# Performance work log

Measured on AMD Instinct MI355X. Metric: run time of the kernel, lower is better.

## Reference

```python
import jax, jax.numpy as jnp
import numpy as np
import math

N, E, H, NB, NL, NG, NELEM = 50000, 800000, 64, 8, 2, 64, 100
CUTOFF = 5.0


def _lin(k, fin, fout):
    kw, kb = jax.random.split(k)
    bound = 1.0 / math.sqrt(fin)
    w = jax.random.uniform(kw, (fin, fout), jnp.float32, -bound, bound)
    b = jax.random.uniform(kb, (fout,), jnp.float32, -bound, bound)
    return w, b


def setup_inputs() -> dict:
    key = jax.random.key(0)
    ks = jax.random.split(key, 12)
    z = jax.random.randint(ks[0], (N,), 0, NELEM)
    pos = jax.random.normal(ks[1], (N, 3), jnp.float32)
    edge_index = jax.random.randint(ks[2], (2, E), 0, N)
    batch = jnp.sort(jax.random.randint(ks[3], (N,), 0, NG))
    embed = jax.random.normal(ks[4], (NELEM, H), jnp.float32)
    # stacked per-interaction MLP params, leading dim = NL
    msg_w1, msg_b1, msg_w2, msg_b2 = [], [], [], []
    upd_w1, upd_b1, upd_w2, upd_b2 = [], [], [], []
    for l in range(NL):
        kl = jax.random.fold_in(ks[5], l)
        k1, k2, k3, k4 = jax.random.split(kl, 4)
        w, b = _lin(k1, 2 * H + NB, H); msg_w1.append(w); msg_b1.append(b)
        w, b = _lin(k2, H, H); msg_w2.append(w); msg_b2.append(b)
        w, b = _lin(k3, 2 * H, H); upd_w1.append(w); upd_b1.append(b)
        w, b = _lin(k4, H, H); upd_w2.append(w); upd_b2.append(b)
    eh_w1, eh_b1 = _lin(ks[6], H, H)
    eh_w2, eh_b2 = _lin(ks[7], H, 1)
    return {
        "z": z, "pos": pos, "edge_index": edge_index, "batch": batch,
        "embed": embed,
        "msg_w1": jnp.stack(msg_w1), "msg_b1": jnp.stack(msg_b1),
        "msg_w2": jnp.stack(msg_w2), "msg_b2": jnp.stack(msg_b2),
        "upd_w1": jnp.stack(upd_w1), "upd_b1": jnp.stack(upd_b1),
        "upd_w2": jnp.stack(upd_w2), "upd_b2": jnp.stack(upd_b2),
        "eh_w1": eh_w1, "eh_b1": eh_b1, "eh_w2": eh_w2, "eh_b2": eh_b2,
    }


def _mace_energy(pos, embed, msg_w1, msg_b1, msg_w2, msg_b2,
                 upd_w1, upd_b1, upd_w2, upd_b2,
                 eh_w1, eh_b1, eh_w2, eh_b2,
                 z, edge_index, batch):
    row, col = edge_index[0], edge_index[1]
    edge_vec = pos[row] - pos[col]                      # (E,3)
    d = jnp.linalg.norm(edge_vec, axis=-1)              # (E,)
    env = jnp.where(d < CUTOFF,
                    jnp.cos(d * (math.pi / (2 * CUTOFF))) ** 2,
                    0.0)
    freqs = jnp.arange(1, NB + 1, dtype=pos.dtype) * (math.pi / CUTOFF)
    d_safe = jnp.where(d > 0, d, 1.0)[:, None]
    edge_attr = jnp.sin(freqs * d[:, None]) / d_safe * env[:, None]  # (E,NB)

    x = embed[z]                                        # (N,H)
    for l in range(NL):
        # PyG source_to_target: x_j = x[row], x_i = x[col], aggregate at col
        msg_in = jnp.concatenate([x[col], x[row], edge_attr], axis=-1)  # (E,2H+NB)
        m = jax.nn.silu(msg_in @ msg_w1[l] + msg_b1[l]) @ msg_w2[l] + msg_b2[l]
        agg = jax.ops.segment_sum(m, col, num_segments=N)               # (N,H)
        u_in = jnp.concatenate([x, agg], axis=-1)
        upd = jax.nn.silu(u_in @ upd_w1[l] + upd_b1[l]) @ upd_w2[l] + upd_b2[l]
        x = x + upd

    atomic_e = jax.nn.silu(x @ eh_w1 + eh_b1) @ eh_w2 + eh_b2           # (N,1)
    energy = jax.ops.segment_sum(atomic_e, batch, num_segments=NG)      # (NG,1)
    return energy.squeeze(-1)


def reference(z, pos, edge_index, batch, embed,
              msg_w1, msg_b1, msg_w2, msg_b2,
              upd_w1, upd_b1, upd_w2, upd_b2,
              eh_w1, eh_b1, eh_w2, eh_b2):
    return _mace_energy(pos, embed, msg_w1, msg_b1, msg_w2, msg_b2,
                        upd_w1, upd_b1, upd_w2, upd_b2,
                        eh_w1, eh_b1, eh_w2, eh_b2,
                        z, edge_index, batch)
```

## Files before the change

kernel.cpp:

```cpp
#include <hip/hip_runtime.h>
#include <math.h>

#define NN 50000
#define EE 800000
#define HH 64
#define NBASIS 8
#define NLAYER 2
#define NGRAPH 64
#define NBLK1 49

using half2_t = decltype(__builtin_amdgcn_cvt_pkrtz(0.0f, 0.0f));
typedef _Float16 f16x8 __attribute__((ext_vector_type(8)));
typedef float f32x4 __attribute__((ext_vector_type(4)));

union U4H8 { uint4 u; f16x8 h; };

__device__ __forceinline__ float silu_f(float v) {
    return v * (1.0f / (1.0f + __expf(-v)));
}

__device__ __forceinline__ unsigned pk2(float a, float b) {
    union { half2_t h; unsigned u; } x;
    x.h = __builtin_amdgcn_cvt_pkrtz(a, b);
    return x.u;
}

__global__ __launch_bounds__(256) void prep_k(
    const int* __restrict__ z, const float* __restrict__ embed,
    float* __restrict__ x, unsigned* __restrict__ xh,
    const float* __restrict__ msg_w1, const float* __restrict__ msg_w2,
    const float* __restrict__ upd_w1, const float* __restrict__ upd_w2,
    const float* __restrict__ eh_w1,
    unsigned* __restrict__ w1t, unsigned* __restrict__ w2t,
    unsigned* __restrict__ w1tu, unsigned* __restrict__ w2tu,
    unsigned* __restrict__ ehw1t,
    const int* __restrict__ ecol, int* __restrict__ deg)
{
    int b = blockIdx.x;
    if (b < 6250) {
        int idx = b * 256 + threadIdx.x;
        int n = idx >> 5;
        int p = idx & 31;
        const float2* er = (const float2*)(embed + ((size_t)z[n] << 6));
        float2 v = er[p];
        ((float2*)x)[idx] = v;
        xh[idx] = pk2(v.x, v.y);
    } else if (b < 6362) {
        int idx = (b - 6250) * 256 + threadIdx.x;
        if (idx < 10240) {
            int l = idx / 5120, rem = idx % 5120;
            int f = rem / 80, kp = rem % 80;
            const float* w = msg_w1 + (size_t)l * 136 * 64;
            unsigned v = 0;
            if (kp < 68) v = pk2(w[(2*kp)*64 + f], w[(2*kp+1)*64 + f]);
            w1t[idx] = v;
        } else if (idx < 14336) {
            int j = idx - 10240;
            int l = j / 2048, rem = j % 2048;
            int n = rem / 32, kp = rem % 32;
            const float* w = msg_w2 + (size_t)l * 64 * 64;
            w2t[j] = pk2(w[(2*kp)*64 + n], w[(2*kp+1)*64 + n]);
        } else if (idx < 22528) {
            int j = idx - 14336;
            int l = j / 4096, rem = j % 4096;
            int f = rem >> 6, kp = rem & 63;
            const float* w = upd_w1 + (size_t)l * 128 * 64;
            w1tu[j] = pk2(w[(2*kp)*64 + f], w[(2*kp+1)*64 + f]);
        } else if (idx < 26624) {
            int j = idx - 22528;
            int l = j / 2048, rem = j % 2048;
            int n = rem / 32, kp = rem % 32;
            const float* w = upd_w2 + (size_t)l * 64 * 64;
            w2tu[j] = pk2(w[(2*kp)*64 + n], w[(2*kp+1)*64 + n]);
        } else if (idx < 28672) {
            int j = idx - 26624;
            int f = j / 32, kp = j % 32;
            ehw1t[j] = pk2(eh_w1[(2*kp)*64 + f], eh_w1[(2*kp+1)*64 + f]);
        }
    } else {
        int e = (b - 6362) * 256 + threadIdx.x;
        if (e < EE) atomicAdd(&deg[ecol[e]], 1);
    }
}

__global__ __launch_bounds__(1024) void scan1_k(
    const int* __restrict__ deg, int* __restrict__ cursor,
    int* __restrict__ bsum)
{
    __shared__ int wsum[16];
    int t = threadIdx.x, lane = t & 63, wave = t >> 6;
    int i = blockIdx.x * 1024 + t;
    int v = (i < NN) ? deg[i] : 0;
    int s = v;
#pragma unroll
    for (int off = 1; off < 64; off <<= 1) {
        int tv = __shfl_up(s, off, 64);
        if (lane >= off) s += tv;
    }
    if (lane == 63) wsum[wave] = s;
    __syncthreads();
    if (wave == 0) {
        int ws = (lane < 16) ? wsum[lane] : 0;
        int ss = ws;
#pragma unroll
        for (int off = 1; off < 16; off <<= 1) {
            int tv = __shfl_up(ss, off, 64);
            if (lane >= off) ss += tv;
        }
        if (lane < 16) wsum[lane] = ss - ws;
    }
    __syncthreads();
    int excl = wsum[wave] + s - v;
    if (i < NN) cursor[i] = excl;
    if (t == 1023) bsum[blockIdx.x] = excl + v;
}

__global__ __launch_bounds__(64) void scan2_k(int* __restrict__ bsum)
{
    int lane = threadIdx.x;
    int v = (lane < NBLK1) ? bsum[lane] : 0;
    int s = v;
#pragma unroll
    for (int off = 1; off < 64; off <<= 1) {
        int tv = __shfl_up(s, off, 64);
        if (lane >= off) s += tv;
    }
    if (lane < NBLK1) bsum[lane] = s - v;
}

__global__ __launch_bounds__(256) void scatter_k(
    const int* __restrict__ erow, const int* __restrict__ ecol,
    const float* __restrict__ pos,
    int* __restrict__ cursor, const int* __restrict__ bsum,
    uint4* __restrict__ edgeS)
{
    int e = blockIdx.x * 256 + threadIdx.x;
    if (e >= EE) return;
    int c = ecol[e], r = erow[e];
    int slot = atomicAdd(&cursor[c], 1) + bsum[c >> 10];
    float dx = pos[3*r]   - pos[3*c];
    float dy = pos[3*r+1] - pos[3*c+1];
    float dz = pos[3*r+2] - pos[3*c+2];
    float d = sqrtf(dx*dx + dy*dy + dz*dz);
    uint4 v;
    v.x = (unsigned)r; v.y = (unsigned)c;
    v.z = __float_as_uint(d); v.w = 0;
    edgeS[slot] = v;
}

__global__ __launch_bounds__(256, 4) void msg_k(
    const uint4* __restrict__ edgeS,
    const unsigned* __restrict__ xh,
    const unsigned* __restrict__ w1t, const float* __restrict__ b1,
    const unsigned* __restrict__ w2t, const float* __restrict__ b2,
    float* __restrict__ agg)
{
    __shared__ __align__(16) unsigned earr[4][64 * 4];
    __shared__ int ckey_s[4][64];
    __shared__ int rkey_s[4][64];
    __shared__ float Mbuf[4][64 * 33];

    const int wid  = threadIdx.x >> 6;
    const int lane = threadIdx.x & 63;
    const int q = lane >> 4, n15 = lane & 15;
    const size_t base = (size_t)blockIdx.x * 256 + wid * 64;

    int mykey;
    {
        uint4 ev = edgeS[base + lane];
        rkey_s[wid][lane] = (int)ev.x;
        mykey = (int)ev.y;
        ckey_s[wid][lane] = mykey;
        float d = __uint_as_float(ev.z);
        float env = 0.0f;
        if (d < 5.0f) {
            float cv = __cosf(d * 0.31415926535897932f);
            env = cv * cv;
        }
        float scale = (d > 0.0f) ? (env / d) : env;
        float ea[NBASIS];
#pragma unroll
        for (int k = 0; k < NBASIS; ++k)
            ea[k] = __sinf((float)(k + 1) * 0.62831853071795865f * d) * scale;
#pragma unroll
        for (int p = 0; p < 4; ++p)
            earr[wid][lane * 4 + p] = pk2(ea[2*p], ea[2*p+1]);
    }
    int pkk = __shfl_up(mykey, 1, 64);
    unsigned long long bmask = __ballot(lane > 0 && mykey != pkk);
    unsigned m32 = (unsigned)(bmask >> (lane & 32));
    __syncthreads();

    int cn[4], rn[4];
#pragma unroll
    for (int nt = 0; nt < 4; ++nt) {
        int eB = nt * 16 + n15;
        cn[nt] = ckey_s[wid][eB];
        rn[nt] = rkey_s[wid][eB];
    }

    f32x4 acc1[4][4];
#pragma unroll
    for (int mt = 0; mt < 4; ++mt) {
        f32x4 binit = *(const f32x4*)(b1 + mt * 16 + q * 4);
#pragma unroll
        for (int nt = 0; nt < 4; ++nt) acc1[mt][nt] = binit;
    }
#pragma unroll
    for (int ks = 0; ks < 5; ++ks) {
        U4H8 bfk[4];
#pragma unroll
        for (int nt = 0; nt < 4; ++nt) {
            if (ks == 4) {
                uint4 zz; zz.x = zz.y = zz.z = zz.w = 0;
                bfk[nt].u = (q == 0) ? *(const uint4*)(earr[wid] + (nt * 16 + n15) * 4) : zz;
            } else if (ks < 2) {
                bfk[nt].u = ((const uint4*)(xh + ((size_t)cn[nt] << 5)))[ks * 4 + q];
            } else {
                bfk[nt].u = ((const uint4*)(xh + ((size_t)rn[nt] << 5)))[(ks - 2) * 4 + q];
            }
        }
#pragma unroll
        for (int mt = 0; mt < 4; ++mt) {
            U4H8 af;
            af.u = *(const uint4*)(w1t + (size_t)(mt * 16 + n15) * 80 + ks * 16 + q * 4);
#pragma unroll
            for (int nt = 0; nt < 4; ++nt)
                acc1[mt][nt] = __builtin_amdgcn_mfma_f32_16x16x32_f16(
                    af.h, bfk[nt].h, acc1[mt][nt], 0, 0, 0);
        }
    }

    unsigned psrc[4][4][2];
#pragma unroll
    for (int mt = 0; mt < 4; ++mt)
#pragma unroll
        for (int nt = 0; nt < 4; ++nt) {
            psrc[mt][nt][0] = pk2(silu_f(acc1[mt][nt][0]), silu_f(acc1[mt][nt][1]));
            psrc[mt][nt][1] = pk2(silu_f(acc1[mt][nt][2]), silu_f(acc1[mt][nt][3]));
        }

    f32x4 acc2[4][4];
#pragma unroll
    for (int nt = 0; nt < 4; ++nt) {
        float b2v = b2[nt * 16 + n15];
        f32x4 binit; binit[0] = b2v; binit[1] = b2v; binit[2] = b2v; binit[3] = b2v;
#pragma unroll
        for (int et = 0; et < 4; ++et) acc2[et][nt] = binit;
    }
#pragma unroll
    for (int ks2 = 0; ks2 < 2; ++ks2) {
        U4H8 wb[4];
#pragma unroll
        for (int nt = 0; nt < 4; ++nt)
            wb[nt].u = *(const uint4*)(w2t + (size_t)(nt * 16 + n15) * 32 + ks2 * 16 + q * 4);
#pragma unroll
        for (int et = 0; et < 4; ++et) {
            unsigned tmp[4];
#pragma unroll
            for (int jr = 0; jr < 4; ++jr) {
                int srcl = (2 * (q & 1) + (jr >> 1)) * 16 + n15;
                unsigned v0 = (unsigned)__shfl((int)psrc[2 * ks2][et][jr & 1], srcl, 64);
                unsigned v1 = (unsigned)__shfl((int)psrc[2 * ks2 + 1][et][jr & 1], srcl, 64);
                tmp[jr] = (q >> 1) ? v1 : v0;
            }
            U4H8 pf;
            pf.u.x = tmp[0]; pf.u.y = tmp[1]; pf.u.z = tmp[2]; pf.u.w = tmp[3];
#pragma unroll
            for (int nt = 0; nt < 4; ++nt)
                acc2[et][nt] = __builtin_amdgcn_mfma_f32_16x16x32_f16(
                    pf.h, wb[nt].h, acc2[et][nt], 0, 0, 0);
        }
    }

#pragma unroll
    for (int hf = 0; hf < 2; ++hf) {
#pragma unroll
        for (int et = 0; et < 4; ++et)
#pragma unroll
            for (int t2 = 0; t2 < 2; ++t2) {
                int nt = 2 * hf + t2;
                int cl = t2 * 16 + n15;
                int eb = et * 16 + q * 4;
#pragma unroll
                for (int r = 0; r < 4; ++r)
                    Mbuf[wid][(eb + r) * 33 + cl] = acc2[et][nt][r];
            }
        __syncthreads();
        {
            int cl = lane & 31, st = lane >> 5;
            int ebase = 32 * st;
            float run = Mbuf[wid][ebase * 33 + cl];
            int runkey = ckey_s[wid][ebase];
            bool atstart = true;
#pragma unroll
            for (int i = 1; i < 32; ++i) {
                float v = Mbuf[wid][(ebase + i) * 33 + cl];
                if ((m32 >> i) & 1u) {
                    float* dst = agg + ((size_t)runkey << 6) + hf * 32 + cl;
                    if (atstart) atomicAdd(dst, run); else *dst = run;
                    runkey = ckey_s[wid][ebase + i]; atstart = false;
                    run = v;
                } else {
                    run += v;
                }
            }
            atomicAdd(agg + ((size_t)runkey << 6) + hf * 32 + cl, run);
        }
        __syncthreads();
    }
}

__global__ __launch_bounds__(256) void upd_k(
    float* __restrict__ x, unsigned* __restrict__ xh,
    float* __restrict__ agg,
    const unsigned* __restrict__ w1t, const float* __restrict__ b1,
    const unsigned* __restrict__ w2t, const float* __restrict__ b2,
    const unsigned* __restrict__ ehw1t, const float* __restrict__ ehb1,
    const float* __restrict__ ehw2, const float* __restrict__ ehb2,
    const int* __restrict__ batch, float* __restrict__ energy,
    int do_zero, int do_head)
{
    __shared__ unsigned MU[4][16 * 33];
    __shared__ float esum[NGRAPH];

    const int tid = threadIdx.x;
    const int wid = tid >> 6;
    const int lane = tid & 63;
    const int q = lane >> 4, n15 = lane & 15;
    const int base16 = blockIdx.x * 64 + wid * 16;

    if (do_head) {
        if (tid < NGRAPH) esum[tid] = 0.0f;
        __syncthreads();
    }

    int nodeB = base16 + n15;
    int ncB = (nodeB < NN) ? nodeB : (NN - 1);

    f32x4 acc1[4];
#pragma unroll
    for (int mt = 0; mt < 4; ++mt)
        acc1[mt] = *(const f32x4*)(b1 + mt * 16 + q * 4);
#pragma unroll
    for (int ks = 0; ks < 4; ++ks) {
        U4H8 bfk;
        if (ks < 2) {
            bfk.u = ((const uint4*)(xh + ((size_t)ncB << 5)))[ks * 4 + q];
        } else {
            const float4* ap = (const float4*)(agg + ((size_t)ncB << 6));
            int o = (ks - 2) * 8 + 2 * q;
            float4 a0 = ap[o], a1 = ap[o + 1];
            bfk.u.x = pk2(a0.x, a0.y); bfk.u.y = pk2(a0.z, a0.w);
            bfk.u.z = pk2(a1.x, a1.y); bfk.u.w = pk2(a1.z, a1.w);
        }
#pragma unroll
        for (int mt = 0; mt < 4; ++mt) {
            U4H8 af;
            af.u = *(const uint4*)(w1t + (size_t)(mt * 16 + n15) * 64 + ks * 16 + q * 4);
            acc1[mt] = __builtin_amdgcn_mfma_f32_16x16x32_f16(
                af.h, bfk.h, acc1[mt], 0, 0, 0);
        }
    }

    unsigned psrc[4][2];
#pragma unroll
    for (int mt = 0; mt < 4; ++mt) {
        psrc[mt][0] = pk2(silu_f(acc1[mt][0]), silu_f(acc1[mt][1]));
        psrc[mt][1] = pk2(silu_f(acc1[mt][2]), silu_f(acc1[mt][3]));
    }

    f32x4 acc2[4];
#pragma unroll
    for (int nt = 0; nt < 4; ++nt) {
        float b2v = b2[nt * 16 + n15];
        acc2[nt][0] = b2v; acc2[nt][1] = b2v; acc2[nt][2] = b2v; acc2[nt][3] = b2v;
    }
#pragma unroll
    for (int ks2 = 0; ks2 < 2; ++ks2) {
        unsigned tmp[4];
#pragma unroll
        for (int jr = 0; jr < 4; ++jr) {
            int srcl = (2 * (q & 1) + (jr >> 1)) * 16 + n15;
            unsigned v0 = (unsigned)__shfl((int)psrc[2 * ks2][jr & 1], srcl, 64);
            unsigned v1 = (unsigned)__shfl((int)psrc[2 * ks2 + 1][jr & 1], srcl, 64);
            tmp[jr] = (q >> 1) ? v1 : v0;
        }
        U4H8 pf;
        pf.u.x = tmp[0]; pf.u.y = tmp[1]; pf.u.z = tmp[2]; pf.u.w = tmp[3];
#pragma unroll
        for (int nt = 0; nt < 4; ++nt) {
            U4H8 wb;
            wb.u = *(const uint4*)(w2t + (size_t)(nt * 16 + n15) * 32 + ks2 * 16 + q * 4);
            acc2[nt] = __builtin_amdgcn_mfma_f32_16x16x32_f16(
                pf.h, wb.h, acc2[nt], 0, 0, 0);
        }
    }

#pragma unroll
    for (int nt = 0; nt < 4; ++nt) {
#pragma unroll
        for (int r = 0; r < 4; ++r) {
            int node = base16 + 4 * q + r;
            float vnew = 0.0f;
            if (node < NN) {
                float* xp = x + ((size_t)node << 6) + nt * 16 + n15;
                vnew = *xp + acc2[nt][r];
                *xp = vnew;
            }
            float vpart = __shfl_xor(vnew, 1, 64);
            if ((n15 & 1) == 0) {
                unsigned pv = pk2(vnew, vpart);
                int pidx = nt * 8 + (n15 >> 1);
                MU[wid][(4 * q + r) * 33 + pidx] = pv;
                if (node < NN) xh[((size_t)node << 5) + pidx] = pv;
            }
        }
    }

    if (do_zero) {
        if (nodeB < NN) {
            float4 z4; z4.x = z4.y = z4.z = z4.w = 0.0f;
            float4* ap = (float4*)(agg + ((size_t)nodeB << 6));
            ap[2*q] = z4; ap[2*q + 1] = z4;
            ap[8 + 2*q] = z4; ap[8 + 2*q + 1] = z4;
        }
    }

    if (do_head) {
        __syncthreads();
        f32x4 acch[4];
#pragma unroll
        for (int mt = 0; mt < 4; ++mt)
            acch[mt] = *(const f32x4*)(ehb1 + mt * 16 + q * 4);
#pragma unroll
        for (int ks = 0; ks < 2; ++ks) {
            U4H8 bfk;
            bfk.u.x = MU[wid][n15 * 33 + ks * 16 + 4 * q + 0];
            bfk.u.y = MU[wid][n15 * 33 + ks * 16 + 4 * q + 1];
            bfk.u.z = MU[wid][n15 * 33 + ks * 16 + 4 * q + 2];
            bfk.u.w = MU[wid][n15 * 33 + ks * 16 + 4 * q + 3];
#pragma unroll
            for (int mt = 0; mt < 4; ++mt) {
                U4H8 af;
                af.u = *(const uint4*)(ehw1t + (size_t)(mt * 16 + n15) * 32 + ks * 16 + q * 4);
                acch[mt] = __builtin_amdgcn_mfma_f32_16x16x32_f16(
                    af.h, bfk.h, acch[mt], 0, 0, 0);
            }
        }
        f32x4 wv[4];
#pragma unroll
        for (int mt = 0; mt < 4; ++mt)
            wv[mt] = *(const f32x4*)(ehw2 + mt * 16 + q * 4);
        float e = 0.0f;
#pragma unroll
        for (int mt = 0; mt < 4; ++mt)
#pragma unroll
            for (int r = 0; r < 4; ++r)
                e = fmaf(silu_f(acch[mt][r]), wv[mt][r], e);
        e += __shfl_xor(e, 16, 64);
        e += __shfl_xor(e, 32, 64);
        if (q == 0) {
            int node = base16 + n15;
            if (node < NN) atomicAdd(&esum[batch[node]], e + ehb2[0]);
        }
        __syncthreads();
        if (tid < NGRAPH) {
            float v = esum[tid];
            if (v != 0.0f) atomicAdd(energy + tid, v);
        }
    }
}

extern "C" void kernel_launch(void* const* d_in, const int* in_sizes, int n_in,
                              void* d_out, int out_size, void* d_ws, size_t ws_size,
                              hipStream_t stream) {
    const int*   z       = (const int*)  d_in[0];
    const float* pos     = (const float*)d_in[1];
    const int*   eidx    = (const int*)  d_in[2];
    const int*   batch   = (const int*)  d_in[3];
    const float* embed   = (const float*)d_in[4];
    const float* msg_w1  = (const float*)d_in[5];
    const float* msg_b1  = (const float*)d_in[6];
    const float* msg_w2  = (const float*)d_in[7];
    const float* msg_b2  = (const float*)d_in[8];
    const float* upd_w1  = (const float*)d_in[9];
    const float* upd_b1  = (const float*)d_in[10];
    const float* upd_w2  = (const float*)d_in[11];
    const float* upd_b2  = (const float*)d_in[12];
    const float* eh_w1   = (const float*)d_in[13];
    const float* eh_b1   = (const float*)d_in[14];
    const float* eh_w2   = (const float*)d_in[15];
    const float* eh_b2   = (const float*)d_in[16];

    const int* erow = eidx;
    const int* ecol = eidx + EE;

    float*    x      = (float*)d_ws;
    float*    agg    = x + (size_t)NN * HH;
    unsigned* xh     = (unsigned*)(agg + (size_t)NN * HH);
    int*      deg    = (int*)(xh + (size_t)NN * 32);
    int*      cursor = deg + NN;
    int*      bsum   = cursor + NN;
    uint4*    edgeS  = (uint4*)(bsum + 64);
    unsigned* w1t    = (unsigned*)(edgeS + EE);
    unsigned* w2t    = w1t + NLAYER * 64 * 80;
    unsigned* w1tu   = w2t + NLAYER * 64 * 32;
    unsigned* w2tu   = w1tu + NLAYER * 64 * 64;
    unsigned* ehw1t  = w2tu + NLAYER * 64 * 32;
    float*    energy = (float*)d_out;

    (void)hipMemsetAsync(energy, 0, NGRAPH * sizeof(float), stream);
    (void)hipMemsetAsync(deg, 0, NN * sizeof(int), stream);
    (void)hipMemsetAsync(agg, 0, (size_t)NN * HH * sizeof(float), stream);

    prep_k<<<9487, 256, 0, stream>>>(
        z, embed, x, xh,
        msg_w1, msg_w2, upd_w1, upd_w2, eh_w1,
        w1t, w2t, w1tu, w2tu, ehw1t,
        ecol, deg);

    scan1_k<<<NBLK1, 1024, 0, stream>>>(deg, cursor, bsum);
    scan2_k<<<1, 64, 0, stream>>>(bsum);
    scatter_k<<<(EE + 255) / 256, 256, 0, stream>>>(
        erow, ecol, pos, cursor, bsum, edgeS);

    for (int l = 0; l < NLAYER; ++l) {
        msg_k<<<EE / 256, 256, 0, stream>>>(
            edgeS, xh,
            w1t + (size_t)l * 64 * 80,
            msg_b1 + (size_t)l * HH,
            w2t + (size_t)l * 64 * 32,
            msg_b2 + (size_t)l * HH,
            agg);
        upd_k<<<(NN + 63) / 64, 256, 0, stream>>>(
            x, xh, agg,
            w1tu + (size_t)l * 64 * 64,
            upd_b1 + (size_t)l * HH,
            w2tu + (size_t)l * 64 * 32,
            upd_b2 + (size_t)l * HH,
            ehw1t, eh_b1, eh_w2, eh_b2, batch, energy,
            (l == 0) ? 1 : 0,
            (l == NLAYER - 1) ? 1 : 0);
    }
}
```

Before: 388.5 us.

## Drop fp32 node state, prefetch row features early, remove block barriers in msg kernel

Removes the fp32 copy of node features x and keeps only the fp16 packed xh, so the residual update in upd_k reads the old value from xh instead of a separate fp32 array. In msg_k, edge row and column indices are now distributed with wave shuffles rather than through shared memory, and the row-node feature gathers are issued early so they overlap with the radial basis computation. The block-wide __syncthreads are removed because each wave only touches its own shared-memory slices. The cost is that the residual stream now accumulates in fp16 across layers, which lowers precision, and the larger prefetch raises register pressure.

```diff
diff --git a/kernel.cpp b/kernel.cpp
--- a/kernel.cpp
+++ b/kernel.cpp
@@ -25,9 +25,13 @@
     return x.u;
 }
 
+__device__ __forceinline__ half2_t u2h(unsigned u) {
+    union { unsigned u; half2_t h; } x; x.u = u; return x.h;
+}
+
 __global__ __launch_bounds__(256) void prep_k(
     const int* __restrict__ z, const float* __restrict__ embed,
-    float* __restrict__ x, unsigned* __restrict__ xh,
+    unsigned* __restrict__ xh,
     const float* __restrict__ msg_w1, const float* __restrict__ msg_w2,
     const float* __restrict__ upd_w1, const float* __restrict__ upd_w2,
     const float* __restrict__ eh_w1,
@@ -43,7 +47,6 @@
         int p = idx & 31;
         const float2* er = (const float2*)(embed + ((size_t)z[n] << 6));
         float2 v = er[p];
-        ((float2*)x)[idx] = v;
         xh[idx] = pk2(v.x, v.y);
     } else if (b < 6362) {
         int idx = (b - 6250) * 256 + threadIdx.x;
@@ -157,7 +160,6 @@
 {
     __shared__ __align__(16) unsigned earr[4][64 * 4];
     __shared__ int ckey_s[4][64];
-    __shared__ int rkey_s[4][64];
     __shared__ float Mbuf[4][64 * 33];
 
     const int wid  = threadIdx.x >> 6;
@@ -165,12 +167,27 @@
     const int q = lane >> 4, n15 = lane & 15;
     const size_t base = (size_t)blockIdx.x * 256 + wid * 64;
 
-    int mykey;
+    uint4 ev = edgeS[base + lane];
+    int myrow = (int)ev.x;
+    int mykey = (int)ev.y;
+    ckey_s[wid][lane] = mykey;
+
+    int cn[4], rn[4];
+#pragma unroll
+    for (int nt = 0; nt < 4; ++nt) {
+        cn[nt] = __shfl(mykey, nt * 16 + n15, 64);
+        rn[nt] = __shfl(myrow, nt * 16 + n15, 64);
+    }
+
+    U4H8 bfr[2][4];
+#pragma unroll
+    for (int nt = 0; nt < 4; ++nt) {
+        const uint4* rp = (const uint4*)(xh + ((size_t)rn[nt] << 5));
+        bfr[0][nt].u = rp[q];
+        bfr[1][nt].u = rp[4 + q];
+    }
+
     {
-        uint4 ev = edgeS[base + lane];
-        rkey_s[wid][lane] = (int)ev.x;
-        mykey = (int)ev.y;
-        ckey_s[wid][lane] = mykey;
         float d = __uint_as_float(ev.z);
         float env = 0.0f;
         if (d < 5.0f) {
@@ -189,15 +206,6 @@
     int pkk = __shfl_up(mykey, 1, 64);
     unsigned long long bmask = __ballot(lane > 0 && mykey != pkk);
     unsigned m32 = (unsigned)(bmask >> (lane & 32));
-    __syncthreads();
-
-    int cn[4], rn[4];
-#pragma unroll
-    for (int nt = 0; nt < 4; ++nt) {
-        int eB = nt * 16 + n15;
-        cn[nt] = ckey_s[wid][eB];
-        rn[nt] = rkey_s[wid][eB];
-    }
 
     f32x4 acc1[4][4];
 #pragma unroll
@@ -217,7 +225,7 @@
             } else if (ks < 2) {
                 bfk[nt].u = ((const uint4*)(xh + ((size_t)cn[nt] << 5)))[ks * 4 + q];
             } else {
-                bfk[nt].u = ((const uint4*)(xh + ((size_t)rn[nt] << 5)))[(ks - 2) * 4 + q];
+                bfk[nt] = bfr[ks - 2][nt];
             }
         }
 #pragma unroll
@@ -286,7 +294,6 @@
                 for (int r = 0; r < 4; ++r)
                     Mbuf[wid][(eb + r) * 33 + cl] = acc2[et][nt][r];
             }
-        __syncthreads();
         {
             int cl = lane & 31, st = lane >> 5;
             int ebase = 32 * st;
@@ -307,12 +314,11 @@
             }
             atomicAdd(agg + ((size_t)runkey << 6) + hf * 32 + cl, run);
         }
-        __syncthreads();
     }
 }
 
 __global__ __launch_bounds__(256) void upd_k(
-    float* __restrict__ x, unsigned* __restrict__ xh,
+    unsigned* __restrict__ xh,
     float* __restrict__ agg,
     const unsigned* __restrict__ w1t, const float* __restrict__ b1,
     const unsigned* __restrict__ w2t, const float* __restrict__ b2,
@@ -404,9 +410,10 @@
             int node = base16 + 4 * q + r;
             float vnew = 0.0f;
             if (node < NN) {
-                float* xp = x + ((size_t)node << 6) + nt * 16 + n15;
-                vnew = *xp + acc2[nt][r];
-                *xp = vnew;
+                unsigned pu = xh[((size_t)node << 5) + (unsigned)((nt * 16 + n15) >> 1)];
+                half2_t hp = u2h(pu);
+                float vold = (n15 & 1) ? (float)hp[1] : (float)hp[0];
+                vnew = vold + acc2[nt][r];
             }
             float vpart = __shfl_xor(vnew, 1, 64);
             if ((n15 & 1) == 0) {
@@ -496,8 +503,7 @@
     const int* erow = eidx;
     const int* ecol = eidx + EE;
 
-    float*    x      = (float*)d_ws;
-    float*    agg    = x + (size_t)NN * HH;
+    float*    agg    = (float*)d_ws;
     unsigned* xh     = (unsigned*)(agg + (size_t)NN * HH);
     int*      deg    = (int*)(xh + (size_t)NN * 32);
     int*      cursor = deg + NN;
@@ -515,7 +521,7 @@
     (void)hipMemsetAsync(agg, 0, (size_t)NN * HH * sizeof(float), stream);
 
     prep_k<<<9487, 256, 0, stream>>>(
-        z, embed, x, xh,
+        z, embed, xh,
         msg_w1, msg_w2, upd_w1, upd_w2, eh_w1,
         w1t, w2t, w1tu, w2tu, ehw1t,
         ecol, deg);
@@ -534,7 +540,7 @@
             msg_b2 + (size_t)l * HH,
             agg);
         upd_k<<<(NN + 63) / 64, 256, 0, stream>>>(
-            x, xh, agg,
+            xh, agg,
             w1tu + (size_t)l * 64 * 64,
             upd_b1 + (size_t)l * HH,
             w2tu + (size_t)l * 64 * 32,
```

Result: no change. 385.0 us (-0.9%).
